# Performance work log

Hardware: AMD Instinct MI355X
Metric: run time of the kernel (lower is better)

## Reference

```python
import jax, jax.numpy as jnp
import numpy as np

N_NODES = 10000
N_EDGES = 20000
N_GRAPHS = 64
DIM = 64
NFEAT = 32
EDIM = 16
NCLS = 10
EPS = 1e-5  # BatchNorm eps (torch default)


def setup_inputs() -> dict:
    key = jax.random.key(0)
    ks = jax.random.split(key, 20)
    def w(k, shape, s=0.05):
        return jax.random.normal(k, shape, dtype=jnp.float32) * s
    z = lambda *s: jnp.zeros(s, jnp.float32)
    inp = {}
    inp["x"] = jax.random.normal(ks[0], (N_NODES, NFEAT), dtype=jnp.float32)
    inp["edge_index"] = jax.random.randint(ks[1], (2, N_EDGES), 0, N_NODES)
    inp["edge_attr"] = jax.random.normal(ks[2], (N_EDGES, EDIM), dtype=jnp.float32)
    inp["batch"] = jax.random.randint(ks[3], (N_NODES,), 0, N_GRAPHS)
    # edge_transform
    inp["et_w"] = w(ks[4], (EDIM, DIM)); inp["et_b"] = z(DIM)
    # conv_in edge-MLP (dim->128->num_features*dim) + root weight + bias
    inp["nn1_w1"] = w(ks[5], (DIM, 128)); inp["nn1_b1"] = z(128)
    inp["nn1_w2"] = w(ks[6], (128, NFEAT * DIM)); inp["nn1_b2"] = z(NFEAT * DIM)
    inp["root_in"] = w(ks[7], (NFEAT, DIM)); inp["bias_in"] = z(DIM)
    # 4 residual NNConv layers, params stacked on leading axis
    inp["convs_w1"] = w(ks[8], (4, DIM, 128)); inp["convs_b1"] = z(4, 128)
    inp["convs_w2"] = w(ks[9], (4, 128, DIM * DIM)); inp["convs_b2"] = z(4, DIM * DIM)
    inp["convs_root"] = w(ks[10], (4, DIM, DIM)); inp["convs_bias"] = z(4, DIM)
    # 5 BatchNorm layers (affine)
    inp["bn_gamma"] = jnp.ones((5, DIM), jnp.float32); inp["bn_beta"] = z(5, DIM)
    # head
    inp["lin1_w"] = w(ks[11], (DIM, DIM)); inp["lin1_b"] = z(DIM)
    inp["lin2_w"] = w(ks[12], (DIM, DIM)); inp["lin2_b"] = z(DIM)
    inp["lout_w"] = w(ks[13], (DIM, NCLS)); inp["lout_b"] = z(NCLS)
    return inp


def _bn(x, g, b):
    # BatchNorm1d training-mode math: biased variance over nodes
    m = x.mean(0)
    v = jnp.mean((x - m) ** 2, 0)
    return g * (x - m) / jnp.sqrt(v + EPS) + b


def _nnconv(x, src, dst, e, w1, b1, w2, b2, root, bias, in_dim):
    # PyG NNConv: per-edge weight matrix from edge MLP, gather->bmm->scatter-add, plus root transform
    h = jax.nn.relu(e @ w1 + b1)                       # [E,128]
    W = (h @ w2 + b2).reshape(-1, in_dim, DIM)         # [E,in,out]
    msg = jnp.einsum('ei,eio->eo', x[src], W)          # [E,out]
    agg = jax.ops.segment_sum(msg, dst, num_segments=N_NODES)
    return agg + x @ root + bias


def reference(x, edge_index, edge_attr, batch,
              et_w, et_b,
              nn1_w1, nn1_b1, nn1_w2, nn1_b2, root_in, bias_in,
              convs_w1, convs_b1, convs_w2, convs_b2, convs_root, convs_bias,
              bn_gamma, bn_beta,
              lin1_w, lin1_b, lin2_w, lin2_b, lout_w, lout_b):
    src, dst = edge_index[0], edge_index[1]
    e = edge_attr @ et_w + et_b                        # [E,DIM]
    h = jax.nn.relu(_bn(
        _nnconv(x, src, dst, e, nn1_w1, nn1_b1, nn1_w2, nn1_b2, root_in, bias_in, NFEAT),
        bn_gamma[0], bn_beta[0]))
    for k in range(4):  # residual NNConv blocks
        h = jax.nn.relu(_bn(
            _nnconv(h, src, dst, e, convs_w1[k], convs_b1[k], convs_w2[k], convs_b2[k],
                    convs_root[k], convs_bias[k], DIM),
            bn_gamma[k + 1], bn_beta[k + 1])) + h
    g = jax.ops.segment_max(h, batch, num_segments=N_GRAPHS)  # global_max_pool
    g = jax.nn.relu(g @ lin1_w + lin1_b)  # dropout = identity (eval/deterministic)
    g = jax.nn.relu(g @ lin2_w + lin2_b)
    return jax.nn.sigmoid(g @ lout_w + lout_b)
```

## Files before the change

kernel.cpp:

```cpp
#include <hip/hip_runtime.h>
#include <hip/hip_bf16.h>
#include <math.h>

#define N_NODES 10000
#define N_EDGES 20000
#define EPAD 20224
#define N_GRAPHS 64
#define DIM 64
#define NFEAT 32
#define EDIM 16
#define NCLS 10

typedef short short8 __attribute__((ext_vector_type(8)));
typedef float f32x16 __attribute__((ext_vector_type(16)));

static __device__ __forceinline__ short f2b(float f) {
  __hip_bfloat16 h = __float2bfloat16(f);
  return __builtin_bit_cast(short, h);
}

static __device__ __forceinline__ void gload_lds16(const void* g, void* s) {
  __builtin_amdgcn_global_load_lds(
      (const __attribute__((address_space(1))) unsigned int*)g,
      (__attribute__((address_space(3))) unsigned int*)s, 16, 0, 0);
}

__global__ __launch_bounds__(256) void k_pack_all(
    const float* __restrict__ w20, const float* __restrict__ b20,
    const float* __restrict__ w2c, const float* __restrict__ b2c,
    short* __restrict__ pk, float* __restrict__ gpool) {
  const int b = blockIdx.x, t = threadIdx.x;
  if (b == 0) { for (int i = t; i < N_GRAPHS * DIM; i += 256) gpool[i] = 0.f; }
  __shared__ float tile[32][65];
  const float *w2, *b2; short* out; int K, lb;
  if (b < 129) { w2 = w20; b2 = b20; out = pk; K = 4096; lb = b; }
  else {
    int bb = b - 129; int k = bb / 258; lb = bb % 258;
    w2 = w2c + (size_t)k * 8192 * 64; b2 = b2c + (size_t)k * 4096;
    out = pk + 264192 + (size_t)k * 528384; K = 8192;
  }
  #pragma unroll
  for (int it = 0; it < 2; ++it) {
    int idx = t + it * 256;
    int r = idx >> 4, c4 = idx & 15;
    int k = lb * 32 + r;
    const float* sp = (k < K) ? (w2 + (size_t)k * 64 + c4 * 4)
                              : (b2 + (size_t)(k - K) * 64 + c4 * 4);
    float4 v = *(const float4*)sp;
    float* dr = &tile[r][c4 * 4];
    dr[0] = v.x; dr[1] = v.y; dr[2] = v.z; dr[3] = v.w;
  }
  __syncthreads();
  const int S_local = t >> 7, n = (t >> 6) & 1, l = t & 63;
  const int rbase = S_local * 16 + ((l >> 5) << 3);
  const int col = n * 32 + (l & 31);
  short8 o;
  #pragma unroll
  for (int u = 0; u < 8; ++u) o[u] = f2b(tile[rbase + u][col]);
  ((short8*)out)[(size_t)lb * 256 + t] = o;
}

__global__ __launch_bounds__(256) void k_ef_mlp1(
    const float* __restrict__ ea, const float* __restrict__ etw,
    const float* __restrict__ etb, const float* __restrict__ w1,
    const float* __restrict__ b1, float* __restrict__ e_feat,
    float* __restrict__ h1) {
  __shared__ float sea[8][17];
  __shared__ float se[8][65];
  const int b = blockIdx.x, t = threadIdx.x;
  const int e0 = b * 8;
  if (t < 128) {
    int r = t >> 4, c = t & 15;
    sea[r][c] = ea[(size_t)(e0 + r) * EDIM + c];
  }
  __syncthreads();
  {
    int o = t & 63, eh = t >> 6;
    #pragma unroll
    for (int k = 0; k < 2; ++k) {
      int r = eh * 2 + k;
      float a = etb[o];
      #pragma unroll
      for (int i = 0; i < EDIM; ++i) a = fmaf(sea[r][i], etw[i * 64 + o], a);
      se[r][o] = a;
      e_feat[(size_t)(e0 + r) * 64 + o] = a;
    }
  }
  __syncthreads();
  {
    int j = t & 127, eh = t >> 7;
    int r0 = eh * 4;
    float a0 = b1[j], a1 = a0, a2 = a0, a3 = a0;
    #pragma unroll 8
    for (int i = 0; i < 64; ++i) {
      float wv = w1[i * 128 + j];
      a0 = fmaf(se[r0 + 0][i], wv, a0);
      a1 = fmaf(se[r0 + 1][i], wv, a1);
      a2 = fmaf(se[r0 + 2][i], wv, a2);
      a3 = fmaf(se[r0 + 3][i], wv, a3);
    }
    size_t base = (size_t)(e0 + r0) * 128 + j;
    h1[base +   0] = fmaxf(a0, 0.f);
    h1[base + 128] = fmaxf(a1, 0.f);
    h1[base + 256] = fmaxf(a2, 0.f);
    h1[base + 384] = fmaxf(a3, 0.f);
  }
}

__global__ __launch_bounds__(256) void k_root0(const float* __restrict__ x,
    const float* __restrict__ rootw, const float* __restrict__ rootb,
    float* __restrict__ agg, double* __restrict__ part0) {
  if (blockIdx.x == 0 && threadIdx.x < 128) part0[threadIdx.x] = 0.0;
  int idx = blockIdx.x * 256 + threadIdx.x;
  if (idx >= N_NODES * DIM) return;
  int n = idx >> 6, o = idx & 63;
  float a = rootb[o];
  const float* hr = x + (size_t)n * NFEAT;
  #pragma unroll 8
  for (int i = 0; i < NFEAT; ++i) a = fmaf(hr[i], rootw[i * 64 + o], a);
  agg[idx] = a;
}

template<int IN>
__global__ __launch_bounds__(256, 2) void k_msg(
    const float* __restrict__ h1, const float* __restrict__ xin,
    const int* __restrict__ src, const short* __restrict__ pk,
    float* __restrict__ pt) {
  constexpr int QW = IN / 16;
  constexpr int JR = 32;
  constexpr int GBYTES = QW * 2048;
  __shared__ float sh_h[256][JR + 1];
  __shared__ __align__(16) short bbuf[2][QW * 1024];
  const int t = threadIdx.x, l = t & 63, w = t >> 6;
  const int e0 = blockIdx.x * 256;
  const int jbase = blockIdx.y * JR;
  const int ng = JR + (blockIdx.y == 0 ? 1 : 0);

  const char* pkc = (const char*)pk;
  const char* bias_gb = pkc + (size_t)(8 * IN) * 2048;

  auto stage = [&](int g) {
    const char* gb = (g < JR) ? pkc + (size_t)(jbase + g) * GBYTES : bias_gb;
    #pragma unroll
    for (int s = 0; s < QW / 2; ++s) {
      int off = w * (GBYTES / 4) + s * 1024;
      gload_lds16(gb + off + l * 16, (char*)&bbuf[g & 1][0] + off);
    }
  };

  #pragma unroll
  for (int it = 0; it < 8; ++it) {
    int idx = t + it * 256;
    int row = idx >> 3, c4 = idx & 7;
    int e = e0 + row;
    float4 v = {0.f, 0.f, 0.f, 0.f};
    if (e < N_EDGES) v = *(const float4*)(h1 + (size_t)e * 128 + jbase + c4 * 4);
    float* dr = &sh_h[row][c4 * 4];
    dr[0] = v.x; dr[1] = v.y; dr[2] = v.z; dr[3] = v.w;
  }
  stage(0);

  const int h8 = (l >> 5) << 3;
  float xr[2][QW][8];
  #pragma unroll
  for (int m = 0; m < 2; ++m) {
    int eme = e0 + w * 64 + m * 32 + (l & 31);
    int srow = src[eme < N_EDGES ? eme : 0];
    #pragma unroll
    for (int q = 0; q < QW; ++q) {
      const float* xp = xin + (size_t)srow * IN + q * 16 + h8;
      float4 a = *(const float4*)xp;
      float4 bq = *(const float4*)(xp + 4);
      xr[m][q][0] = a.x;  xr[m][q][1] = a.y;  xr[m][q][2] = a.z;  xr[m][q][3] = a.w;
      xr[m][q][4] = bq.x; xr[m][q][5] = bq.y; xr[m][q][6] = bq.z; xr[m][q][7] = bq.w;
    }
  }

  f32x16 acc00 = {}, acc01 = {}, acc10 = {}, acc11 = {};

  for (int g = 0; g < ng; ++g) {
    asm volatile("s_waitcnt vmcnt(0)" ::: "memory");
    __syncthreads();
    if (g + 1 < ng) stage(g + 1);
    const short8* bp = (const short8*)&bbuf[g & 1][0];
    if (g < JR) {
      float hv0 = sh_h[w * 64 + (l & 31)][g];
      float hv1 = sh_h[w * 64 + 32 + (l & 31)][g];
      #pragma unroll
      for (int q = 0; q < QW; ++q) {
        short8 b0 = bp[q * 128 + l];
        short8 b1 = bp[q * 128 + 64 + l];
        short8 av0, av1;
        #pragma unroll
        for (int u = 0; u < 8; ++u) {
          av0[u] = f2b(hv0 * xr[0][q][u]);
          av1[u] = f2b(hv1 * xr[1][q][u]);
        }
        acc00 = __builtin_amdgcn_mfma_f32_32x32x16_bf16(av0, b0, acc00, 0, 0, 0);
        acc01 = __builtin_amdgcn_mfma_f32_32x32x16_bf16(av0, b1, acc01, 0, 0, 0);
        acc10 = __builtin_amdgcn_mfma_f32_32x32x16_bf16(av1, b0, acc10, 0, 0, 0);
        acc11 = __builtin_amdgcn_mfma_f32_32x32x16_bf16(av1, b1, acc11, 0, 0, 0);
      }
    } else {
      #pragma unroll
      for (int q = 0; q < QW; ++q) {
        short8 b0 = bp[q * 128 + l];
        short8 b1 = bp[q * 128 + 64 + l];
        short8 av0, av1;
        #pragma unroll
        for (int u = 0; u < 8; ++u) {
          av0[u] = f2b(xr[0][q][u]);
          av1[u] = f2b(xr[1][q][u]);
        }
        acc00 = __builtin_amdgcn_mfma_f32_32x32x16_bf16(av0, b0, acc00, 0, 0, 0);
        acc01 = __builtin_amdgcn_mfma_f32_32x32x16_bf16(av0, b1, acc01, 0, 0, 0);
        acc10 = __builtin_amdgcn_mfma_f32_32x32x16_bf16(av1, b0, acc10, 0, 0, 0);
        acc11 = __builtin_amdgcn_mfma_f32_32x32x16_bf16(av1, b1, acc11, 0, 0, 0);
      }
    }
  }

  float* po = pt + ((size_t)blockIdx.y * EPAD + e0 + w * 64) * 64 + (l & 31);
  #pragma unroll
  for (int v = 0; v < 16; ++v) {
    int r = (v & 3) + ((v >> 2) << 3) + ((l >> 5) << 2);
    po[(size_t)r * 64]             = acc00[v];
    po[(size_t)r * 64 + 32]       = acc01[v];
    po[(size_t)(r + 32) * 64]      = acc10[v];
    po[(size_t)(r + 32) * 64 + 32] = acc11[v];
  }
}

__global__ __launch_bounds__(256) void k_reduce(const float* __restrict__ pt,
    const int* __restrict__ dst, float* __restrict__ agg) {
  int idx = blockIdx.x * 256 + threadIdx.x;
  int e = idx >> 4;
  if (e >= N_EDGES) return;
  int c = (idx & 15) * 4;
  const float* p = pt + (size_t)e * 64 + c;
  float4 s0 = *(const float4*)p;
  float4 s1 = *(const float4*)(p + (size_t)EPAD * 64);
  float4 s2 = *(const float4*)(p + (size_t)2 * EPAD * 64);
  float4 s3 = *(const float4*)(p + (size_t)3 * EPAD * 64);
  float* ap = agg + (size_t)dst[e] * 64 + c;
  atomicAdd(ap + 0, s0.x + s1.x + s2.x + s3.x);
  atomicAdd(ap + 1, s0.y + s1.y + s2.y + s3.y);
  atomicAdd(ap + 2, s0.z + s1.z + s2.z + s3.z);
  atomicAdd(ap + 3, s0.w + s1.w + s2.w + s3.w);
}

__global__ __launch_bounds__(256) void k_bnpart(const float* __restrict__ agg,
    double* __restrict__ part) {
  const int t = threadIdx.x;
  const int c = t & 63, rg = t >> 6;
  const int r0 = blockIdx.x * 50;
  const int r1 = min(r0 + 50, N_NODES);
  double s = 0.0, s2 = 0.0;
  for (int r = r0 + rg; r < r1; r += 4) {
    float v = agg[(size_t)r * 64 + c];
    s += v;
    s2 += (double)v * v;
  }
  __shared__ double shs[4][64];
  __shared__ double shq[4][64];
  shs[rg][c] = s; shq[rg][c] = s2;
  __syncthreads();
  if (t < 64) {
    double ts = shs[0][t] + shs[1][t] + shs[2][t] + shs[3][t];
    double tq = shq[0][t] + shq[1][t] + shq[2][t] + shq[3][t];
    atomicAdd(&part[t], ts);
    atomicAdd(&part[64 + t], tq);
  }
}

__global__ __launch_bounds__(256) void k_inter(
    const float* __restrict__ agg, const double* __restrict__ part,
    const float* __restrict__ gamma, const float* __restrict__ beta,
    const float* resid, float* __restrict__ hout,
    const float* __restrict__ rootw, const float* __restrict__ rootb,
    float* __restrict__ aggn, double* __restrict__ partn,
    const float* __restrict__ ef, const float* __restrict__ w1,
    const float* __restrict__ b1, float* __restrict__ h1) {
  const int b = blockIdx.x, t = threadIdx.x;
  if (b < 157) {
    __shared__ float sh[64][65];
    if (b == 0 && t < 128) partn[t] = 0.0;
    const int o = t & 63, rg = t >> 6;
    const int n0 = b * 64;
    float m = (float)(part[o] * (1.0 / N_NODES));
    float s2 = (float)(part[64 + o] * (1.0 / N_NODES));
    float inv = 1.0f / sqrtf(s2 - m * m + 1e-5f);
    float sc = gamma[o] * inv;
    float sf = beta[o] - m * sc;
    #pragma unroll
    for (int k = 0; k < 16; ++k) {
      int r = rg * 16 + k;
      int n = n0 + r;
      float v = 0.f;
      if (n < N_NODES) {
        v = fmaxf(fmaf(agg[(size_t)n * 64 + o], sc, sf), 0.f);
        if (resid) v += resid[(size_t)n * 64 + o];
        hout[(size_t)n * 64 + o] = v;
      }
      sh[r][o] = v;
    }
    __syncthreads();
    float acc[16];
    float rb = rootb[o];
    #pragma unroll
    for (int k = 0; k < 16; ++k) acc[k] = rb;
    for (int i = 0; i < 64; ++i) {
      float wv = rootw[i * 64 + o];
      #pragma unroll
      for (int k = 0; k < 16; ++k) acc[k] = fmaf(sh[rg * 16 + k][i], wv, acc[k]);
    }
    #pragma unroll
    for (int k = 0; k < 16; ++k) {
      int n = n0 + rg * 16 + k;
      if (n < N_NODES) aggn[(size_t)n * 64 + o] = acc[k];
    }
  } else {
    const int e0 = (b - 157) * 8;
    __shared__ float se[8][65];
    {
      int r = t >> 5, ci = (t & 31) * 2;
      const float* sp = ef + (size_t)(e0 + r) * 64 + ci;
      se[r][ci] = sp[0];
      se[r][ci + 1] = sp[1];
    }
    __syncthreads();
    const int j = t & 127, eh = t >> 7;
    const int r0 = eh * 4;
    float a0 = b1[j], a1 = a0, a2 = a0, a3 = a0;
    #pragma unroll 8
    for (int i = 0; i < 64; ++i) {
      float wv = w1[i * 128 + j];
      a0 = fmaf(se[r0 + 0][i], wv, a0);
      a1 = fmaf(se[r0 + 1][i], wv, a1);
      a2 = fmaf(se[r0 + 2][i], wv, a2);
      a3 = fmaf(se[r0 + 3][i], wv, a3);
    }
    size_t base = (size_t)(e0 + r0) * 128 + j;
    h1[base +   0] = fmaxf(a0, 0.f);
    h1[base + 128] = fmaxf(a1, 0.f);
    h1[base + 256] = fmaxf(a2, 0.f);
    h1[base + 384] = fmaxf(a3, 0.f);
  }
}

__global__ __launch_bounds__(256) void k_final(const float* __restrict__ agg,
    const double* __restrict__ part, const float* __restrict__ gamma,
    const float* __restrict__ beta, const float* __restrict__ resid,
    const int* __restrict__ batch, float* __restrict__ gpool) {
  int idx = blockIdx.x * 256 + threadIdx.x;
  if (idx >= N_NODES * DIM) return;
  int c = idx & 63, r = idx >> 6;
  float m = (float)(part[c] * (1.0 / N_NODES));
  float s2 = (float)(part[64 + c] * (1.0 / N_NODES));
  float inv = 1.0f / sqrtf(s2 - m * m + 1e-5f);
  float sc = gamma[c] * inv;
  float sf = beta[c] - m * sc;
  float v = fmaxf(fmaf(agg[idx], sc, sf), 0.f) + resid[idx];
  atomicMax((unsigned int*)&gpool[batch[r] * 64 + c], __float_as_uint(v));
}

__global__ __launch_bounds__(64) void k_head(const float* __restrict__ g,
    const float* __restrict__ w1, const float* __restrict__ b1,
    const float* __restrict__ w2, const float* __restrict__ b2,
    const float* __restrict__ wo, const float* __restrict__ bo,
    float* __restrict__ out) {
  __shared__ float s0[64];
  __shared__ float s1[64];
  const int r = blockIdx.x, t = threadIdx.x;
  s0[t] = g[r * 64 + t];
  __syncthreads();
  float a = b1[t];
  #pragma unroll 8
  for (int i = 0; i < 64; ++i) a = fmaf(s0[i], w1[i * 64 + t], a);
  s1[t] = fmaxf(a, 0.f);
  __syncthreads();
  a = b2[t];
  #pragma unroll 8
  for (int i = 0; i < 64; ++i) a = fmaf(s1[i], w2[i * 64 + t], a);
  __syncthreads();
  s0[t] = fmaxf(a, 0.f);
  __syncthreads();
  if (t < NCLS) {
    float o = bo[t];
    #pragma unroll 8
    for (int i = 0; i < 64; ++i) o = fmaf(s0[i], wo[i * NCLS + t], o);
    out[r * NCLS + t] = 1.f / (1.f + expf(-o));
  }
}

extern "C" void kernel_launch(void* const* d_in, const int* in_sizes, int n_in,
                              void* d_out, int out_size, void* d_ws, size_t ws_size,
                              hipStream_t stream) {
  const float* x          = (const float*)d_in[0];
  const int*   eidx       = (const int*)d_in[1];
  const float* eattr      = (const float*)d_in[2];
  const int*   batch      = (const int*)d_in[3];
  const float* et_w       = (const float*)d_in[4];
  const float* et_b       = (const float*)d_in[5];
  const float* nn1_w1     = (const float*)d_in[6];
  const float* nn1_b1     = (const float*)d_in[7];
  const float* nn1_w2     = (const float*)d_in[8];
  const float* nn1_b2     = (const float*)d_in[9];
  const float* root_in    = (const float*)d_in[10];
  const float* bias_in    = (const float*)d_in[11];
  const float* convs_w1   = (const float*)d_in[12];
  const float* convs_b1   = (const float*)d_in[13];
  const float* convs_w2   = (const float*)d_in[14];
  const float* convs_b2   = (const float*)d_in[15];
  const float* convs_root = (const float*)d_in[16];
  const float* convs_bias = (const float*)d_in[17];
  const float* bn_gamma   = (const float*)d_in[18];
  const float* bn_beta    = (const float*)d_in[19];
  const float* lin1_w     = (const float*)d_in[20];
  const float* lin1_b     = (const float*)d_in[21];
  const float* lin2_w     = (const float*)d_in[22];
  const float* lin2_b     = (const float*)d_in[23];
  const float* lout_w     = (const float*)d_in[24];
  const float* lout_b     = (const float*)d_in[25];

  const int* srcp = eidx;
  const int* dstp = eidx + N_EDGES;

  double* part0 = (double*)d_ws;
  double* part1 = part0 + 128;
  float* e_feat = (float*)(part0 + 256);
  float* h1     = e_feat + N_EDGES * DIM;
  float* agg    = h1 + N_EDGES * 128;
  float* h_cur  = agg + N_NODES * DIM;
  float* g      = h_cur + N_NODES * DIM;
  short* pk0    = (short*)(g + N_GRAPHS * DIM);
  short* pkL[4];
  for (int k = 0; k < 4; ++k) pkL[k] = pk0 + 264192 + (size_t)k * 528384;
  float* pt     = (float*)(pk0 + 264192 + 4 * 528384);
  double* parts[2] = {part0, part1};

  const dim3 gMsg(79, 4);
  const int gRed = EPAD * 16 / 256;

  k_pack_all<<<1161, 256, 0, stream>>>(nn1_w2, nn1_b2, convs_w2, convs_b2, pk0, g);
  k_ef_mlp1<<<2500, 256, 0, stream>>>(eattr, et_w, et_b, nn1_w1, nn1_b1,
                                      e_feat, h1);
  k_root0<<<2500, 256, 0, stream>>>(x, root_in, bias_in, agg, part0);

  k_msg<NFEAT><<<gMsg, 256, 0, stream>>>(h1, x, srcp, pk0, pt);
  k_reduce<<<gRed, 256, 0, stream>>>(pt, dstp, agg);
  k_bnpart<<<200, 256, 0, stream>>>(agg, part0);

  for (int k = 0; k < 4; ++k) {
    k_inter<<<2657, 256, 0, stream>>>(
        agg, parts[k & 1], bn_gamma + k * 64, bn_beta + k * 64,
        (k == 0) ? nullptr : h_cur, h_cur,
        convs_root + (size_t)k * 4096, convs_bias + (size_t)k * 64,
        agg, parts[(k + 1) & 1],
        e_feat, convs_w1 + (size_t)k * 64 * 128, convs_b1 + (size_t)k * 128, h1);
    k_msg<DIM><<<gMsg, 256, 0, stream>>>(h1, h_cur, srcp, pkL[k], pt);
    k_reduce<<<gRed, 256, 0, stream>>>(pt, dstp, agg);
    k_bnpart<<<200, 256, 0, stream>>>(agg, parts[(k + 1) & 1]);
  }

  k_final<<<2500, 256, 0, stream>>>(agg, parts[0], bn_gamma + 4 * 64,
                                    bn_beta + 4 * 64, h_cur, batch, g);
  k_head<<<N_GRAPHS, 64, 0, stream>>>(g, lin1_w, lin1_b, lin2_w, lin2_b,
                                      lout_w, lout_b, (float*)d_out);
}
```

Measured before the change: 444.6 us.

## Fuse layer kernels into persistent grid-synced combo kernel, transpose h1, triple-buffer B

Merges the pack, edge-MLP and root kernels into one launch, and fuses reduce, BN-stats, inter-layer work and the final pool/head into a persistent 512-block kernel that uses atomic-counter grid barriers. h1 is stored transposed so the message kernel loads it coalesced. The message kernel can split the hidden dimension into 8 chunks when the workspace allows, and it prefetches B tiles two steps ahead with triple buffering and partial vmcnt waits. The intent is to cut launch count and inter-kernel gaps and to add parallelism in the message stage. In exchange, the software grid barrier can deadlock if not all 512 blocks are co-resident, and the 8-chunk split doubles the partial-sum traffic in the reduce.

```diff
diff --git a/kernel.cpp b/kernel.cpp
--- a/kernel.cpp
+++ b/kernel.cpp
@@ -10,6 +10,9 @@
 #define NFEAT 32
 #define EDIM 16
 #define NCLS 10
+#define CGRID 512
+
+static_assert(EPAD == 79 * 256, "EPAD");
 
 typedef short short8 __attribute__((ext_vector_type(8)));
 typedef float f32x16 __attribute__((ext_vector_type(16)));
@@ -25,112 +28,128 @@
       (__attribute__((address_space(3))) unsigned int*)s, 16, 0, 0);
 }
 
-__global__ __launch_bounds__(256) void k_pack_all(
+static __device__ __forceinline__ void gsync(unsigned* bar, int slot) {
+  __syncthreads();
+  if (threadIdx.x == 0) {
+    __threadfence();
+    unsigned prev = __hip_atomic_fetch_add(&bar[slot], 1u, __ATOMIC_ACQ_REL,
+                                           __HIP_MEMORY_SCOPE_AGENT);
+    if (prev + 1u < (unsigned)CGRID) {
+      while (__hip_atomic_load(&bar[slot], __ATOMIC_RELAXED,
+                               __HIP_MEMORY_SCOPE_AGENT) < (unsigned)CGRID)
+        __builtin_amdgcn_s_sleep(8);
+    }
+    __threadfence();
+  }
+  __syncthreads();
+}
+
+__global__ __launch_bounds__(256) void k_pre(
+    const float* __restrict__ ea, const float* __restrict__ etw,
+    const float* __restrict__ etb, const float* __restrict__ nw1,
+    const float* __restrict__ nb1, const float* __restrict__ x,
+    const float* __restrict__ rootw, const float* __restrict__ rootb,
     const float* __restrict__ w20, const float* __restrict__ b20,
     const float* __restrict__ w2c, const float* __restrict__ b2c,
-    short* __restrict__ pk, float* __restrict__ gpool) {
+    float* __restrict__ e_feat, float* __restrict__ h1T,
+    float* __restrict__ agg, double* __restrict__ part0,
+    short* __restrict__ pk, float* __restrict__ gpool,
+    unsigned* __restrict__ bar) {
   const int b = blockIdx.x, t = threadIdx.x;
-  if (b == 0) { for (int i = t; i < N_GRAPHS * DIM; i += 256) gpool[i] = 0.f; }
-  __shared__ float tile[32][65];
-  const float *w2, *b2; short* out; int K, lb;
-  if (b < 129) { w2 = w20; b2 = b20; out = pk; K = 4096; lb = b; }
-  else {
-    int bb = b - 129; int k = bb / 258; lb = bb % 258;
-    w2 = w2c + (size_t)k * 8192 * 64; b2 = b2c + (size_t)k * 4096;
-    out = pk + 264192 + (size_t)k * 528384; K = 8192;
-  }
-  #pragma unroll
-  for (int it = 0; it < 2; ++it) {
-    int idx = t + it * 256;
-    int r = idx >> 4, c4 = idx & 15;
-    int k = lb * 32 + r;
-    const float* sp = (k < K) ? (w2 + (size_t)k * 64 + c4 * 4)
-                              : (b2 + (size_t)(k - K) * 64 + c4 * 4);
-    float4 v = *(const float4*)sp;
-    float* dr = &tile[r][c4 * 4];
-    dr[0] = v.x; dr[1] = v.y; dr[2] = v.z; dr[3] = v.w;
-  }
-  __syncthreads();
-  const int S_local = t >> 7, n = (t >> 6) & 1, l = t & 63;
-  const int rbase = S_local * 16 + ((l >> 5) << 3);
-  const int col = n * 32 + (l & 31);
-  short8 o;
-  #pragma unroll
-  for (int u = 0; u < 8; ++u) o[u] = f2b(tile[rbase + u][col]);
-  ((short8*)out)[(size_t)lb * 256 + t] = o;
-}
-
-__global__ __launch_bounds__(256) void k_ef_mlp1(
-    const float* __restrict__ ea, const float* __restrict__ etw,
-    const float* __restrict__ etb, const float* __restrict__ w1,
-    const float* __restrict__ b1, float* __restrict__ e_feat,
-    float* __restrict__ h1) {
-  __shared__ float sea[8][17];
-  __shared__ float se[8][65];
-  const int b = blockIdx.x, t = threadIdx.x;
-  const int e0 = b * 8;
-  if (t < 128) {
-    int r = t >> 4, c = t & 15;
-    sea[r][c] = ea[(size_t)(e0 + r) * EDIM + c];
-  }
-  __syncthreads();
-  {
-    int o = t & 63, eh = t >> 6;
+  if (b < 1161) {
+    if (b == 0) {
+      for (int i = t; i < N_GRAPHS * DIM; i += 256) gpool[i] = 0.f;
+      if (t < 16) bar[t] = 0u;
+    }
+    __shared__ float tile[32][65];
+    const float *w2, *b2; short* out; int K, lb;
+    if (b < 129) { w2 = w20; b2 = b20; out = pk; K = 4096; lb = b; }
+    else {
+      int bb = b - 129; int k = bb / 258; lb = bb % 258;
+      w2 = w2c + (size_t)k * 8192 * 64; b2 = b2c + (size_t)k * 4096;
+      out = pk + 264192 + (size_t)k * 528384; K = 8192;
+    }
     #pragma unroll
-    for (int k = 0; k < 2; ++k) {
-      int r = eh * 2 + k;
-      float a = etb[o];
+    for (int it = 0; it < 2; ++it) {
+      int idx = t + it * 256;
+      int r = idx >> 4, c4 = idx & 15;
+      int k = lb * 32 + r;
+      const float* sp = (k < K) ? (w2 + (size_t)k * 64 + c4 * 4)
+                                : (b2 + (size_t)(k - K) * 64 + c4 * 4);
+      float4 v = *(const float4*)sp;
+      float* dr = &tile[r][c4 * 4];
+      dr[0] = v.x; dr[1] = v.y; dr[2] = v.z; dr[3] = v.w;
+    }
+    __syncthreads();
+    const int S_local = t >> 7, n = (t >> 6) & 1, l = t & 63;
+    const int rbase = S_local * 16 + ((l >> 5) << 3);
+    const int col = n * 32 + (l & 31);
+    short8 o;
+    #pragma unroll
+    for (int u = 0; u < 8; ++u) o[u] = f2b(tile[rbase + u][col]);
+    ((short8*)out)[(size_t)lb * 256 + t] = o;
+  } else if (b < 3661) {
+    const int e0 = (b - 1161) * 8;
+    __shared__ float sea[8][17];
+    __shared__ float se[8][65];
+    if (t < 128) {
+      int r = t >> 4, c = t & 15;
+      sea[r][c] = ea[(size_t)(e0 + r) * EDIM + c];
+    }
+    __syncthreads();
+    {
+      int o = t & 63, eh = t >> 6;
       #pragma unroll
-      for (int i = 0; i < EDIM; ++i) a = fmaf(sea[r][i], etw[i * 64 + o], a);
-      se[r][o] = a;
-      e_feat[(size_t)(e0 + r) * 64 + o] = a;
-    }
-  }
-  __syncthreads();
-  {
-    int j = t & 127, eh = t >> 7;
-    int r0 = eh * 4;
-    float a0 = b1[j], a1 = a0, a2 = a0, a3 = a0;
-    #pragma unroll 8
-    for (int i = 0; i < 64; ++i) {
-      float wv = w1[i * 128 + j];
-      a0 = fmaf(se[r0 + 0][i], wv, a0);
-      a1 = fmaf(se[r0 + 1][i], wv, a1);
-      a2 = fmaf(se[r0 + 2][i], wv, a2);
-      a3 = fmaf(se[r0 + 3][i], wv, a3);
-    }
-    size_t base = (size_t)(e0 + r0) * 128 + j;
-    h1[base +   0] = fmaxf(a0, 0.f);
-    h1[base + 128] = fmaxf(a1, 0.f);
-    h1[base + 256] = fmaxf(a2, 0.f);
-    h1[base + 384] = fmaxf(a3, 0.f);
-  }
-}
-
-__global__ __launch_bounds__(256) void k_root0(const float* __restrict__ x,
-    const float* __restrict__ rootw, const float* __restrict__ rootb,
-    float* __restrict__ agg, double* __restrict__ part0) {
-  if (blockIdx.x == 0 && threadIdx.x < 128) part0[threadIdx.x] = 0.0;
-  int idx = blockIdx.x * 256 + threadIdx.x;
-  if (idx >= N_NODES * DIM) return;
-  int n = idx >> 6, o = idx & 63;
-  float a = rootb[o];
-  const float* hr = x + (size_t)n * NFEAT;
-  #pragma unroll 8
-  for (int i = 0; i < NFEAT; ++i) a = fmaf(hr[i], rootw[i * 64 + o], a);
-  agg[idx] = a;
-}
-
-template<int IN>
+      for (int k = 0; k < 2; ++k) {
+        int r = eh * 2 + k;
+        float a = etb[o];
+        #pragma unroll
+        for (int i = 0; i < EDIM; ++i) a = fmaf(sea[r][i], etw[i * 64 + o], a);
+        se[r][o] = a;
+        e_feat[(size_t)(e0 + r) * 64 + o] = a;
+      }
+    }
+    __syncthreads();
+    {
+      int j = t & 127, eh = t >> 7;
+      int r0 = eh * 4;
+      float a0 = nb1[j], a1 = a0, a2 = a0, a3 = a0;
+      #pragma unroll 8
+      for (int i = 0; i < 64; ++i) {
+        float wv = nw1[i * 128 + j];
+        a0 = fmaf(se[r0 + 0][i], wv, a0);
+        a1 = fmaf(se[r0 + 1][i], wv, a1);
+        a2 = fmaf(se[r0 + 2][i], wv, a2);
+        a3 = fmaf(se[r0 + 3][i], wv, a3);
+      }
+      float4 o = {fmaxf(a0, 0.f), fmaxf(a1, 0.f), fmaxf(a2, 0.f), fmaxf(a3, 0.f)};
+      *(float4*)(h1T + (size_t)j * EPAD + e0 + r0) = o;
+    }
+  } else {
+    const int u = b - 3661;
+    if (u == 0 && t < 128) part0[t] = 0.0;
+    int idx = u * 256 + t;
+    if (idx < N_NODES * DIM) {
+      int n = idx >> 6, o = idx & 63;
+      float a = rootb[o];
+      const float* hr = x + (size_t)n * NFEAT;
+      #pragma unroll 8
+      for (int i = 0; i < NFEAT; ++i) a = fmaf(hr[i], rootw[i * 64 + o], a);
+      agg[idx] = a;
+    }
+  }
+}
+
+template<int IN, int NC>
 __global__ __launch_bounds__(256, 2) void k_msg(
-    const float* __restrict__ h1, const float* __restrict__ xin,
+    const float* __restrict__ h1T, const float* __restrict__ xin,
     const int* __restrict__ src, const short* __restrict__ pk,
     float* __restrict__ pt) {
   constexpr int QW = IN / 16;
-  constexpr int JR = 32;
-  constexpr int GBYTES = QW * 2048;
+  constexpr int JR = 128 / NC;
+  constexpr int GB = QW * 2048;
   __shared__ float sh_h[256][JR + 1];
-  __shared__ __align__(16) short bbuf[2][QW * 1024];
+  __shared__ __align__(16) short bbuf[3][QW * 1024];
   const int t = threadIdx.x, l = t & 63, w = t >> 6;
   const int e0 = blockIdx.x * 256;
   const int jbase = blockIdx.y * JR;
@@ -140,25 +159,24 @@
   const char* bias_gb = pkc + (size_t)(8 * IN) * 2048;
 
   auto stage = [&](int g) {
-    const char* gb = (g < JR) ? pkc + (size_t)(jbase + g) * GBYTES : bias_gb;
+    const char* gb = (g < JR) ? pkc + (size_t)(jbase + g) * GB : bias_gb;
     #pragma unroll
     for (int s = 0; s < QW / 2; ++s) {
-      int off = w * (GBYTES / 4) + s * 1024;
-      gload_lds16(gb + off + l * 16, (char*)&bbuf[g & 1][0] + off);
+      int off = w * (QW * 512) + s * 1024;
+      gload_lds16(gb + off + l * 16, (char*)&bbuf[g % 3][0] + off);
     }
   };
 
   #pragma unroll
-  for (int it = 0; it < 8; ++it) {
-    int idx = t + it * 256;
-    int row = idx >> 3, c4 = idx & 7;
-    int e = e0 + row;
-    float4 v = {0.f, 0.f, 0.f, 0.f};
-    if (e < N_EDGES) v = *(const float4*)(h1 + (size_t)e * 128 + jbase + c4 * 4);
-    float* dr = &sh_h[row][c4 * 4];
-    dr[0] = v.x; dr[1] = v.y; dr[2] = v.z; dr[3] = v.w;
-  }
-  stage(0);
+  for (int it = 0; it < JR / 4; ++it) {
+    int u = t + it * 256;
+    int jj = u >> 6, c4 = u & 63;
+    float4 v = *(const float4*)(h1T + (size_t)(jbase + jj) * EPAD + e0 + c4 * 4);
+    sh_h[c4 * 4 + 0][jj] = v.x;
+    sh_h[c4 * 4 + 1][jj] = v.y;
+    sh_h[c4 * 4 + 2][jj] = v.z;
+    sh_h[c4 * 4 + 3][jj] = v.w;
+  }
 
   const int h8 = (l >> 5) << 3;
   float xr[2][QW][8];
@@ -176,13 +194,22 @@
     }
   }
 
+  asm volatile("s_waitcnt vmcnt(0) lgkmcnt(0)" ::: "memory");
+  stage(0);
+  if (ng > 1) stage(1);
+
   f32x16 acc00 = {}, acc01 = {}, acc10 = {}, acc11 = {};
 
   for (int g = 0; g < ng; ++g) {
-    asm volatile("s_waitcnt vmcnt(0)" ::: "memory");
-    __syncthreads();
-    if (g + 1 < ng) stage(g + 1);
-    const short8* bp = (const short8*)&bbuf[g & 1][0];
+    if (g + 1 < ng) {
+      if constexpr (QW / 2 == 2) asm volatile("s_waitcnt vmcnt(2)" ::: "memory");
+      else                       asm volatile("s_waitcnt vmcnt(1)" ::: "memory");
+    } else {
+      asm volatile("s_waitcnt vmcnt(0)" ::: "memory");
+    }
+    asm volatile("s_barrier" ::: "memory");
+    if (g + 2 < ng) stage(g + 2);
+    const short8* bp = (const short8*)&bbuf[g % 3][0];
     if (g < JR) {
       float hv0 = sh_h[w * 64 + (l & 31)][g];
       float hv1 = sh_h[w * 64 + 32 + (l & 31)][g];
@@ -225,171 +252,181 @@
   for (int v = 0; v < 16; ++v) {
     int r = (v & 3) + ((v >> 2) << 3) + ((l >> 5) << 2);
     po[(size_t)r * 64]             = acc00[v];
-    po[(size_t)r * 64 + 32]       = acc01[v];
+    po[(size_t)r * 64 + 32]        = acc01[v];
     po[(size_t)(r + 32) * 64]      = acc10[v];
     po[(size_t)(r + 32) * 64 + 32] = acc11[v];
   }
 }
 
-__global__ __launch_bounds__(256) void k_reduce(const float* __restrict__ pt,
-    const int* __restrict__ dst, float* __restrict__ agg) {
-  int idx = blockIdx.x * 256 + threadIdx.x;
-  int e = idx >> 4;
-  if (e >= N_EDGES) return;
-  int c = (idx & 15) * 4;
-  const float* p = pt + (size_t)e * 64 + c;
-  float4 s0 = *(const float4*)p;
-  float4 s1 = *(const float4*)(p + (size_t)EPAD * 64);
-  float4 s2 = *(const float4*)(p + (size_t)2 * EPAD * 64);
-  float4 s3 = *(const float4*)(p + (size_t)3 * EPAD * 64);
-  float* ap = agg + (size_t)dst[e] * 64 + c;
-  atomicAdd(ap + 0, s0.x + s1.x + s2.x + s3.x);
-  atomicAdd(ap + 1, s0.y + s1.y + s2.y + s3.y);
-  atomicAdd(ap + 2, s0.z + s1.z + s2.z + s3.z);
-  atomicAdd(ap + 3, s0.w + s1.w + s2.w + s3.w);
-}
-
-__global__ __launch_bounds__(256) void k_bnpart(const float* __restrict__ agg,
-    double* __restrict__ part) {
+__global__ __launch_bounds__(256, 4) void k_combo(
+    const float* __restrict__ pt, int nc, const int* __restrict__ dst,
+    float* __restrict__ agg, const double* __restrict__ part,
+    const float* __restrict__ gamma, const float* __restrict__ beta,
+    const float* resid, float* __restrict__ h_cur,
+    const float* __restrict__ rootw, const float* __restrict__ rootb,
+    double* __restrict__ partn, double* __restrict__ partw,
+    const float* __restrict__ ef, const float* __restrict__ w1,
+    const float* __restrict__ b1, float* __restrict__ h1T,
+    unsigned* bar, int bar_base, int mode,
+    const int* __restrict__ batch, float* __restrict__ gpool,
+    const float* __restrict__ hw1, const float* __restrict__ hb1,
+    const float* __restrict__ hw2, const float* __restrict__ hb2,
+    const float* __restrict__ hwo, const float* __restrict__ hbo,
+    float* __restrict__ out) {
   const int t = threadIdx.x;
-  const int c = t & 63, rg = t >> 6;
-  const int r0 = blockIdx.x * 50;
-  const int r1 = min(r0 + 50, N_NODES);
-  double s = 0.0, s2 = 0.0;
-  for (int r = r0 + rg; r < r1; r += 4) {
-    float v = agg[(size_t)r * 64 + c];
-    s += v;
-    s2 += (double)v * v;
-  }
+  __shared__ float sh[64][65];
   __shared__ double shs[4][64];
   __shared__ double shq[4][64];
-  shs[rg][c] = s; shq[rg][c] = s2;
-  __syncthreads();
-  if (t < 64) {
-    double ts = shs[0][t] + shs[1][t] + shs[2][t] + shs[3][t];
-    double tq = shq[0][t] + shq[1][t] + shq[2][t] + shq[3][t];
-    atomicAdd(&part[t], ts);
-    atomicAdd(&part[64 + t], tq);
-  }
-}
-
-__global__ __launch_bounds__(256) void k_inter(
-    const float* __restrict__ agg, const double* __restrict__ part,
-    const float* __restrict__ gamma, const float* __restrict__ beta,
-    const float* resid, float* __restrict__ hout,
-    const float* __restrict__ rootw, const float* __restrict__ rootb,
-    float* __restrict__ aggn, double* __restrict__ partn,
-    const float* __restrict__ ef, const float* __restrict__ w1,
-    const float* __restrict__ b1, float* __restrict__ h1) {
-  const int b = blockIdx.x, t = threadIdx.x;
-  if (b < 157) {
-    __shared__ float sh[64][65];
-    if (b == 0 && t < 128) partn[t] = 0.0;
-    const int o = t & 63, rg = t >> 6;
-    const int n0 = b * 64;
-    float m = (float)(part[o] * (1.0 / N_NODES));
-    float s2 = (float)(part[64 + o] * (1.0 / N_NODES));
-    float inv = 1.0f / sqrtf(s2 - m * m + 1e-5f);
-    float sc = gamma[o] * inv;
-    float sf = beta[o] - m * sc;
-    #pragma unroll
-    for (int k = 0; k < 16; ++k) {
-      int r = rg * 16 + k;
-      int n = n0 + r;
-      float v = 0.f;
-      if (n < N_NODES) {
-        v = fmaxf(fmaf(agg[(size_t)n * 64 + o], sc, sf), 0.f);
-        if (resid) v += resid[(size_t)n * 64 + o];
-        hout[(size_t)n * 64 + o] = v;
-      }
-      sh[r][o] = v;
-    }
+  __shared__ float se[8][65];
+  __shared__ float hs0[64];
+  __shared__ float hs1[64];
+
+  for (int u = blockIdx.x; u < (EPAD * 16) / 256; u += CGRID) {
+    int idx = u * 256 + t;
+    int e = idx >> 4;
+    int c = (idx & 15) << 2;
+    if (e < N_EDGES) {
+      const float* p = pt + (size_t)e * 64 + c;
+      float4 a = *(const float4*)p;
+      for (int s = 1; s < nc; ++s) {
+        float4 bq = *(const float4*)(p + (size_t)s * EPAD * 64);
+        a.x += bq.x; a.y += bq.y; a.z += bq.z; a.w += bq.w;
+      }
+      float* ap = agg + (size_t)dst[e] * 64 + c;
+      atomicAdd(ap + 0, a.x);
+      atomicAdd(ap + 1, a.y);
+      atomicAdd(ap + 2, a.z);
+      atomicAdd(ap + 3, a.w);
+    }
+  }
+  gsync(bar, bar_base + 0);
+
+  for (int u = blockIdx.x; u < 200; u += CGRID) {
+    const int c = t & 63, rg = t >> 6;
+    const int r0 = u * 50;
+    const int r1 = min(r0 + 50, N_NODES);
+    double s = 0.0, s2 = 0.0;
+    for (int r = r0 + rg; r < r1; r += 4) {
+      float v = agg[(size_t)r * 64 + c];
+      s += v;
+      s2 += (double)v * v;
+    }
+    shs[rg][c] = s; shq[rg][c] = s2;
     __syncthreads();
-    float acc[16];
-    float rb = rootb[o];
-    #pragma unroll
-    for (int k = 0; k < 16; ++k) acc[k] = rb;
-    for (int i = 0; i < 64; ++i) {
-      float wv = rootw[i * 64 + o];
-      #pragma unroll
-      for (int k = 0; k < 16; ++k) acc[k] = fmaf(sh[rg * 16 + k][i], wv, acc[k]);
-    }
-    #pragma unroll
-    for (int k = 0; k < 16; ++k) {
-      int n = n0 + rg * 16 + k;
-      if (n < N_NODES) aggn[(size_t)n * 64 + o] = acc[k];
+    if (t < 64) {
+      double ts = shs[0][t] + shs[1][t] + shs[2][t] + shs[3][t];
+      double tq = shq[0][t] + shq[1][t] + shq[2][t] + shq[3][t];
+      atomicAdd(&partw[t], ts);
+      atomicAdd(&partw[64 + t], tq);
+    }
+    __syncthreads();
+  }
+  gsync(bar, bar_base + 1);
+
+  if (mode == 0) {
+    for (int u = blockIdx.x; u < 2657; u += CGRID) {
+      if (u < 157) {
+        if (u == 0 && t < 128) partn[t] = 0.0;
+        const int o = t & 63, rg = t >> 6;
+        const int n0 = u * 64;
+        float m = (float)(part[o] * (1.0 / N_NODES));
+        float s2 = (float)(part[64 + o] * (1.0 / N_NODES));
+        float inv = 1.0f / sqrtf(s2 - m * m + 1e-5f);
+        float sc = gamma[o] * inv;
+        float sf = beta[o] - m * sc;
+        #pragma unroll
+        for (int k = 0; k < 16; ++k) {
+          int r = rg * 16 + k;
+          int n = n0 + r;
+          float v = 0.f;
+          if (n < N_NODES) {
+            v = fmaxf(fmaf(agg[(size_t)n * 64 + o], sc, sf), 0.f);
+            if (resid) v += resid[(size_t)n * 64 + o];
+            h_cur[(size_t)n * 64 + o] = v;
+          }
+          sh[r][o] = v;
+        }
+        __syncthreads();
+        float acc[16];
+        float rb = rootb[o];
+        #pragma unroll
+        for (int k = 0; k < 16; ++k) acc[k] = rb;
+        for (int i = 0; i < 64; ++i) {
+          float wv = rootw[i * 64 + o];
+          #pragma unroll
+          for (int k = 0; k < 16; ++k) acc[k] = fmaf(sh[rg * 16 + k][i], wv, acc[k]);
+        }
+        #pragma unroll
+        for (int k = 0; k < 16; ++k) {
+          int n = n0 + rg * 16 + k;
+          if (n < N_NODES) agg[(size_t)n * 64 + o] = acc[k];
+        }
+        __syncthreads();
+      } else {
+        const int e0 = (u - 157) * 8;
+        {
+          int r = t >> 5, ci = (t & 31) * 2;
+          const float* sp = ef + (size_t)(e0 + r) * 64 + ci;
+          se[r][ci] = sp[0];
+          se[r][ci + 1] = sp[1];
+        }
+        __syncthreads();
+        const int j = t & 127, eh = t >> 7;
+        const int r0 = eh * 4;
+        float a0 = b1[j], a1 = a0, a2 = a0, a3 = a0;
+        #pragma unroll 8
+        for (int i = 0; i < 64; ++i) {
+          float wv = w1[i * 128 + j];
+          a0 = fmaf(se[r0 + 0][i], wv, a0);
+          a1 = fmaf(se[r0 + 1][i], wv, a1);
+          a2 = fmaf(se[r0 + 2][i], wv, a2);
+          a3 = fmaf(se[r0 + 3][i], wv, a3);
+        }
+        float4 o = {fmaxf(a0, 0.f), fmaxf(a1, 0.f), fmaxf(a2, 0.f), fmaxf(a3, 0.f)};
+        *(float4*)(h1T + (size_t)j * EPAD + e0 + r0) = o;
+        __syncthreads();
+      }
     }
   } else {
-    const int e0 = (b - 157) * 8;
-    __shared__ float se[8][65];
-    {
-      int r = t >> 5, ci = (t & 31) * 2;
-      const float* sp = ef + (size_t)(e0 + r) * 64 + ci;
-      se[r][ci] = sp[0];
-      se[r][ci + 1] = sp[1];
-    }
-    __syncthreads();
-    const int j = t & 127, eh = t >> 7;
-    const int r0 = eh * 4;
-    float a0 = b1[j], a1 = a0, a2 = a0, a3 = a0;
-    #pragma unroll 8
-    for (int i = 0; i < 64; ++i) {
-      float wv = w1[i * 128 + j];
-      a0 = fmaf(se[r0 + 0][i], wv, a0);
-      a1 = fmaf(se[r0 + 1][i], wv, a1);
-      a2 = fmaf(se[r0 + 2][i], wv, a2);
-      a3 = fmaf(se[r0 + 3][i], wv, a3);
-    }
-    size_t base = (size_t)(e0 + r0) * 128 + j;
-    h1[base +   0] = fmaxf(a0, 0.f);
-    h1[base + 128] = fmaxf(a1, 0.f);
-    h1[base + 256] = fmaxf(a2, 0.f);
-    h1[base + 384] = fmaxf(a3, 0.f);
-  }
-}
-
-__global__ __launch_bounds__(256) void k_final(const float* __restrict__ agg,
-    const double* __restrict__ part, const float* __restrict__ gamma,
-    const float* __restrict__ beta, const float* __restrict__ resid,
-    const int* __restrict__ batch, float* __restrict__ gpool) {
-  int idx = blockIdx.x * 256 + threadIdx.x;
-  if (idx >= N_NODES * DIM) return;
-  int c = idx & 63, r = idx >> 6;
-  float m = (float)(part[c] * (1.0 / N_NODES));
-  float s2 = (float)(part[64 + c] * (1.0 / N_NODES));
-  float inv = 1.0f / sqrtf(s2 - m * m + 1e-5f);
-  float sc = gamma[c] * inv;
-  float sf = beta[c] - m * sc;
-  float v = fmaxf(fmaf(agg[idx], sc, sf), 0.f) + resid[idx];
-  atomicMax((unsigned int*)&gpool[batch[r] * 64 + c], __float_as_uint(v));
-}
-
-__global__ __launch_bounds__(64) void k_head(const float* __restrict__ g,
-    const float* __restrict__ w1, const float* __restrict__ b1,
-    const float* __restrict__ w2, const float* __restrict__ b2,
-    const float* __restrict__ wo, const float* __restrict__ bo,
-    float* __restrict__ out) {
-  __shared__ float s0[64];
-  __shared__ float s1[64];
-  const int r = blockIdx.x, t = threadIdx.x;
-  s0[t] = g[r * 64 + t];
-  __syncthreads();
-  float a = b1[t];
-  #pragma unroll 8
-  for (int i = 0; i < 64; ++i) a = fmaf(s0[i], w1[i * 64 + t], a);
-  s1[t] = fmaxf(a, 0.f);
-  __syncthreads();
-  a = b2[t];
-  #pragma unroll 8
-  for (int i = 0; i < 64; ++i) a = fmaf(s1[i], w2[i * 64 + t], a);
-  __syncthreads();
-  s0[t] = fmaxf(a, 0.f);
-  __syncthreads();
-  if (t < NCLS) {
-    float o = bo[t];
-    #pragma unroll 8
-    for (int i = 0; i < 64; ++i) o = fmaf(s0[i], wo[i * NCLS + t], o);
-    out[r * NCLS + t] = 1.f / (1.f + expf(-o));
+    for (int u = blockIdx.x; u < 2500; u += CGRID) {
+      int idx = u * 256 + t;
+      int c = idx & 63, r = idx >> 6;
+      float m = (float)(part[c] * (1.0 / N_NODES));
+      float s2 = (float)(part[64 + c] * (1.0 / N_NODES));
+      float inv = 1.0f / sqrtf(s2 - m * m + 1e-5f);
+      float sc = gamma[c] * inv;
+      float sf = beta[c] - m * sc;
+      float v = fmaxf(fmaf(agg[idx], sc, sf), 0.f) + resid[idx];
+      atomicMax((unsigned int*)&gpool[batch[r] * 64 + c], __float_as_uint(v));
+    }
+    gsync(bar, bar_base + 2);
+    for (int u = blockIdx.x; u < 64; u += CGRID) {
+      if (t < 64) hs0[t] = gpool[u * 64 + t];
+      __syncthreads();
+      float a = 0.f;
+      if (t < 64) {
+        a = hb1[t];
+        #pragma unroll 8
+        for (int i = 0; i < 64; ++i) a = fmaf(hs0[i], hw1[i * 64 + t], a);
+        hs1[t] = fmaxf(a, 0.f);
+      }
+      __syncthreads();
+      if (t < 64) {
+        a = hb2[t];
+        #pragma unroll 8
+        for (int i = 0; i < 64; ++i) a = fmaf(hs1[i], hw2[i * 64 + t], a);
+      }
+      __syncthreads();
+      if (t < 64) hs0[t] = fmaxf(a, 0.f);
+      __syncthreads();
+      if (t < NCLS) {
+        float o = hbo[t];
+        #pragma unroll 8
+        for (int i = 0; i < 64; ++i) o = fmaf(hs0[i], hwo[i * NCLS + t], o);
+        out[u * NCLS + t] = 1.f / (1.f + expf(-o));
+      }
+      __syncthreads();
+    }
   }
 }
 
@@ -426,45 +463,55 @@
   const int* srcp = eidx;
   const int* dstp = eidx + N_EDGES;
 
-  double* part0 = (double*)d_ws;
-  double* part1 = part0 + 128;
-  float* e_feat = (float*)(part0 + 256);
-  float* h1     = e_feat + N_EDGES * DIM;
-  float* agg    = h1 + N_EDGES * 128;
-  float* h_cur  = agg + N_NODES * DIM;
-  float* g      = h_cur + N_NODES * DIM;
-  short* pk0    = (short*)(g + N_GRAPHS * DIM);
+  char* wsb = (char*)d_ws;
+  double* part0 = (double*)wsb;
+  double* part1 = (double*)(wsb + 1024);
+  unsigned* bar = (unsigned*)(wsb + 2048);
+  float* e_feat = (float*)(wsb + 4096);
+  float* h1T    = e_feat + N_EDGES * 64;
+  float* agg    = h1T + 128 * EPAD;
+  float* h_cur  = agg + N_NODES * 64;
+  float* g      = h_cur + N_NODES * 64;
+  short* pk0    = (short*)(g + N_GRAPHS * 64);
   short* pkL[4];
   for (int k = 0; k < 4; ++k) pkL[k] = pk0 + 264192 + (size_t)k * 528384;
   float* pt     = (float*)(pk0 + 264192 + 4 * 528384);
   double* parts[2] = {part0, part1};
 
-  const dim3 gMsg(79, 4);
-  const int gRed = EPAD * 16 / 256;
-
-  k_pack_all<<<1161, 256, 0, stream>>>(nn1_w2, nn1_b2, convs_w2, convs_b2, pk0, g);
-  k_ef_mlp1<<<2500, 256, 0, stream>>>(eattr, et_w, et_b, nn1_w1, nn1_b1,
-                                      e_feat, h1);
-  k_root0<<<2500, 256, 0, stream>>>(x, root_in, bias_in, agg, part0);
-
-  k_msg<NFEAT><<<gMsg, 256, 0, stream>>>(h1, x, srcp, pk0, pt);
-  k_reduce<<<gRed, 256, 0, stream>>>(pt, dstp, agg);
-  k_bnpart<<<200, 256, 0, stream>>>(agg, part0);
+  const size_t base_bytes = (size_t)((char*)pt - wsb);
+  const int nc = (ws_size >= base_bytes + 8ull * EPAD * 64 * 4) ? 8 : 4;
+
+  k_pre<<<6161, 256, 0, stream>>>(eattr, et_w, et_b, nn1_w1, nn1_b1, x,
+                                  root_in, bias_in, nn1_w2, nn1_b2,
+                                  convs_w2, convs_b2, e_feat, h1T, agg,
+                                  part0, pk0, g, bar);
+
+  if (nc == 8) k_msg<32, 8><<<dim3(79, 8), 256, 0, stream>>>(h1T, x, srcp, pk0, pt);
+  else         k_msg<32, 4><<<dim3(79, 4), 256, 0, stream>>>(h1T, x, srcp, pk0, pt);
 
   for (int k = 0; k < 4; ++k) {
-    k_inter<<<2657, 256, 0, stream>>>(
-        agg, parts[k & 1], bn_gamma + k * 64, bn_beta + k * 64,
+    k_combo<<<CGRID, 256, 0, stream>>>(
+        pt, nc, dstp, agg, parts[k & 1], bn_gamma + k * 64, bn_beta + k * 64,
         (k == 0) ? nullptr : h_cur, h_cur,
         convs_root + (size_t)k * 4096, convs_bias + (size_t)k * 64,
-        agg, parts[(k + 1) & 1],
-        e_feat, convs_w1 + (size_t)k * 64 * 128, convs_b1 + (size_t)k * 128, h1);
-    k_msg<DIM><<<gMsg, 256, 0, stream>>>(h1, h_cur, srcp, pkL[k], pt);
-    k_reduce<<<gRed, 256, 0, stream>>>(pt, dstp, agg);
-    k_bnpart<<<200, 256, 0, stream>>>(agg, parts[(k + 1) & 1]);
-  }
-
-  k_final<<<2500, 256, 0, stream>>>(agg, parts[0], bn_gamma + 4 * 64,
-                                    bn_beta + 4 * 64, h_cur, batch, g);
-  k_head<<<N_GRAPHS, 64, 0, stream>>>(g, lin1_w, lin1_b, lin2_w, lin2_b,
-                                      lout_w, lout_b, (float*)d_out);
-}
+        parts[(k + 1) & 1], parts[k & 1],
+        e_feat, convs_w1 + (size_t)k * 8192, convs_b1 + (size_t)k * 128, h1T,
+        bar, k * 3, 0,
+        nullptr, nullptr, nullptr, nullptr, nullptr, nullptr, nullptr, nullptr,
+        nullptr);
+    if (nc == 8) k_msg<64, 8><<<dim3(79, 8), 256, 0, stream>>>(h1T, h_cur, srcp,
+                                                               pkL[k], pt);
+    else         k_msg<64, 4><<<dim3(79, 4), 256, 0, stream>>>(h1T, h_cur, srcp,
+                                                               pkL[k], pt);
+  }
+
+  k_combo<<<CGRID, 256, 0, stream>>>(
+      pt, nc, dstp, agg, parts[0], bn_gamma + 4 * 64, bn_beta + 4 * 64,
+      h_cur, h_cur,
+      nullptr, nullptr, nullptr, parts[0],
+      nullptr, nullptr, nullptr, nullptr,
+      bar, 12, 1,
+      batch, g,
+      lin1_w, lin1_b, lin2_w, lin2_b, lout_w, lout_b,
+      (float*)d_out);
+}
```

Measured after the change: 1.127 ms. 2.53x slower.
